# Kernel tuning notes

Hardware: AMD Instinct MI355X
Metric: run time of the kernel (lower is better)

Reference implementation:

```python
import jax, jax.numpy as jnp
import numpy as np

BLOCK_DIM = 32
INPUT_DIM = 1024
N_BLOCKS = INPUT_DIM // BLOCK_DIM  # 32
HIDDEN = 2 * BLOCK_DIM             # 64
GAPS = [1, 32]                     # block_dim**i for i in range(num_layers=2)


def setup_inputs() -> dict:
    key = jax.random.key(0)
    ks = jax.random.split(key, 9)
    s = 1.0 / np.sqrt(BLOCK_DIM)
    sh = 1.0 / np.sqrt(HIDDEN)
    return {
        "x": jax.random.normal(ks[0], (16384, INPUT_DIM), dtype=jnp.float32),
        # facto net 0: BlockLinear(32, 32, 64) -> ELU -> BlockLinear(32, 64, 32)
        "W1a": jax.random.uniform(ks[1], (N_BLOCKS, BLOCK_DIM, HIDDEN), jnp.float32, -s, s),
        "b1a": jax.random.uniform(ks[2], (N_BLOCKS, HIDDEN), jnp.float32, -s, s),
        "W2a": jax.random.uniform(ks[3], (N_BLOCKS, HIDDEN, BLOCK_DIM), jnp.float32, -sh, sh),
        "b2a": jax.random.uniform(ks[4], (N_BLOCKS, BLOCK_DIM), jnp.float32, -sh, sh),
        # facto net 1
        "W1b": jax.random.uniform(ks[5], (N_BLOCKS, BLOCK_DIM, HIDDEN), jnp.float32, -s, s),
        "b1b": jax.random.uniform(ks[6], (N_BLOCKS, HIDDEN), jnp.float32, -s, s),
        "W2b": jax.random.uniform(ks[7], (N_BLOCKS, HIDDEN, BLOCK_DIM), jnp.float32, -sh, sh),
        "b2b": jax.random.uniform(ks[8], (N_BLOCKS, BLOCK_DIM), jnp.float32, -sh, sh),
    }


def _block_res_mlp(x, W1, b1, W2, b2):
    # x: (bs, input_dim) -> (n_blocks, bs, block_dim)
    bs = x.shape[0]
    xb = x.reshape(bs, N_BLOCKS, BLOCK_DIM).transpose(1, 0, 2)
    h = jax.nn.elu(jnp.einsum('nbi,nio->nbo', xb, W1) + b1[:, None, :])
    h = jnp.einsum('nbi,nio->nbo', h, W2) + b2[:, None, :]
    yb = h + xb  # residual
    return yb.transpose(1, 0, 2).reshape(bs, -1)


def reference(x, W1a, b1a, W2a, b2a, W1b, b1b, W2b, b2b):
    bs = x.shape[0]
    params = [(W1a, b1a, W2a, b2a), (W1b, b1b, W2b, b2b)]
    y = x
    for gap, (W1, b1, W2, b2) in zip(GAPS, params):
        # strided mixing permutation before the block MLP
        y = y.reshape(-1, BLOCK_DIM, gap).transpose(0, 2, 1).reshape(bs, -1)
        y = _block_res_mlp(y, W1, b1, W2, b2)
        # inverse permutation
        y = y.reshape(-1, gap, BLOCK_DIM).transpose(0, 2, 1)
    return y.reshape(bs, -1)
```

## Files before the change

### kernel.cpp

```cpp
#include <hip/hip_runtime.h>


typedef unsigned short u16t;
typedef __bf16 bf16x8 __attribute__((ext_vector_type(8)));
typedef __bf16 bf16x4 __attribute__((ext_vector_type(4)));
typedef float f32x4 __attribute__((ext_vector_type(4)));

__device__ __forceinline__ u16t f2b(float f) {
  union { float f; unsigned u; } v; v.f = f;
  unsigned r = v.u + 0x7FFFu + ((v.u >> 16) & 1u);
  return (u16t)(r >> 16);
}
__device__ __forceinline__ float b2f(u16t h) {
  union { unsigned u; float f; } v; v.u = ((unsigned)h) << 16;
  return v.f;
}
__device__ __forceinline__ u16t f2b_hw(float f) {
  union { __bf16 h; u16t u; } v; v.h = (__bf16)f;
  return v.u;
}
__device__ __forceinline__ float elu(float v) {
  return fmaxf(v, 0.f) + fminf(__expf(v) - 1.f, 0.f);
}

__device__ __forceinline__ int swz(int idx) {
  return idx ^ ((((idx >> 6) ^ (idx >> 10)) & 15) << 2);
}

__global__ __launch_bounds__(256) void pack_weights(
    const float* __restrict__ W1a, const float* __restrict__ W2a,
    const float* __restrict__ W1b, const float* __restrict__ W2b,
    u16t* __restrict__ pW1, u16t* __restrict__ pW2) {
  int tidg = blockIdx.x * 256 + threadIdx.x;
  int tensor = tidg >> 14;
  int r  = tidg & 16383;
  int L  = r >> 13;
  int r2 = r & 8191;
  int n    = r2 >> 8;
  int f    = (r2 >> 6) & 3;
  int lane = r2 & 63;
  int q = lane >> 4, t = lane & 15;

  union { u16t us[8]; uint4 v; } w;
  if (tensor == 0) {
    const float* src = L ? W1b : W1a;
#pragma unroll
    for (int j = 0; j < 8; j++)
      w.us[j] = f2b(src[n * 2048 + (q * 8 + j) * 64 + f * 16 + t]);
    *(uint4*)(pW1 + (size_t)((((L * 32 + n) * 4 + f) * 64 + lane) * 8)) = w.v;
  } else {
    const float* src = L ? W2b : W2a;
    int e = f >> 1, c2 = f & 1;
#pragma unroll
    for (int j = 0; j < 8; j++) {
      int feat = 32 * e + (j >= 4 ? 16 : 0) + 4 * q + (j & 3);
      w.us[j] = f2b(src[n * 2048 + feat * 32 + 16 * c2 + t]);
    }
    *(uint4*)(pW2 + (size_t)((((L * 32 + n) * 4 + f) * 64 + lane) * 8)) = w.v;
  }
}

template <int L>
__device__ __forceinline__ void compute_layer(
    const bf16x8* __restrict__ afr, u16t* __restrict__ tile,
    const u16t* __restrict__ pW1, const u16t* __restrict__ pW2,
    const float* __restrict__ b1, const float* __restrict__ b2,
    int n0, int lane, int q, int t, const bf16x8* __restrict__ ifr) {
#pragma unroll
  for (int u = 0; u < 8; u++) {
    const int n = n0 + u;
    const int wbase = ((L * 32 + n) * 4) * 512 + lane * 8;

    bf16x8 bfrag[2];
#pragma unroll
    for (int e = 0; e < 2; e++) {
      bf16x8 w1lo = *(const bf16x8*)(pW1 + wbase + (2 * e) * 512);
      bf16x8 w1hi = *(const bf16x8*)(pW1 + wbase + (2 * e + 1) * 512);
      f32x4 b1lo = *(const f32x4*)(b1 + n * 64 + (2 * e) * 16 + q * 4);
      f32x4 b1hi = *(const f32x4*)(b1 + n * 64 + (2 * e + 1) * 16 + q * 4);
      f32x4 h0 = __builtin_amdgcn_mfma_f32_16x16x32_bf16(w1lo, afr[u], b1lo, 0, 0, 0);
      f32x4 h1 = __builtin_amdgcn_mfma_f32_16x16x32_bf16(w1hi, afr[u], b1hi, 0, 0, 0);
      bf16x4 a0, a1;
#pragma unroll
      for (int r = 0; r < 4; r++) {
        a0[r] = (__bf16)elu(h0[r]);
        a1[r] = (__bf16)elu(h1[r]);
      }
      bfrag[e] = __builtin_shufflevector(a0, a1, 0, 1, 2, 3, 4, 5, 6, 7);
    }

#pragma unroll
    for (int c2 = 0; c2 < 2; c2++) {
      f32x4 b2v = *(const f32x4*)(b2 + n * 32 + c2 * 16 + q * 4);
      f32x4 acc = __builtin_amdgcn_mfma_f32_16x16x32_bf16(ifr[c2], afr[u], b2v, 0, 0, 0);
#pragma unroll
      for (int e = 0; e < 2; e++) {
        bf16x8 w2f = *(const bf16x8*)(pW2 + wbase + (e * 2 + c2) * 512);
        acc = __builtin_amdgcn_mfma_f32_16x16x32_bf16(w2f, bfrag[e], acc, 0, 0, 0);
      }
#pragma unroll
      for (int r = 0; r < 4; r++) {
        int cc  = c2 * 16 + q * 4 + r;
        int idx = cc * 512 + t * 32 + n;
        tile[swz(idx)] = f2b_hw(acc[r]);
      }
    }
  }
}

__global__ __launch_bounds__(256, 2) void mixer_kernel(
    const float* __restrict__ x,
    const float* __restrict__ b1a, const float* __restrict__ b2a,
    const float* __restrict__ b1b, const float* __restrict__ b2b,
    const u16t* __restrict__ pW1, const u16t* __restrict__ pW2,
    float* __restrict__ out) {
  __shared__ u16t tile[16384];

  const int tid  = threadIdx.x;
  const int wave = tid >> 6, lane = tid & 63;
  const int q = lane >> 4, t = lane & 15;
  const int r0 = blockIdx.x * 16;
  const int n0 = wave * 8;

  bf16x8 ifr[2];
#pragma unroll
  for (int c2 = 0; c2 < 2; c2++) {
    union { u16t us[8]; bf16x8 v; } w;
#pragma unroll
    for (int j = 0; j < 8; j++)
      w.us[j] = ((q * 8 + j) == (c2 * 16 + t)) ? (u16t)0x3F80 : (u16t)0;
    ifr[c2] = w.v;
  }

  bf16x8 afr[8];
#pragma unroll
  for (int u = 0; u < 8; u++) {
    const float* gp = x + (size_t)(r0 + t) * 1024 + (n0 + u) * 32 + q * 8;
    float4 v0 = *(const float4*)gp;
    float4 v1 = *(const float4*)(gp + 4);
    union { __bf16 h[8]; bf16x8 v; } a;
    a.h[0] = (__bf16)v0.x; a.h[1] = (__bf16)v0.y; a.h[2] = (__bf16)v0.z; a.h[3] = (__bf16)v0.w;
    a.h[4] = (__bf16)v1.x; a.h[5] = (__bf16)v1.y; a.h[6] = (__bf16)v1.z; a.h[7] = (__bf16)v1.w;
    afr[u] = a.v;
  }

  compute_layer<0>(afr, tile, pW1, pW2, b1a, b2a, n0, lane, q, t, ifr);
  __syncthreads();

#pragma unroll
  for (int u = 0; u < 8; u++) {
    const int n2 = n0 + u;
    int idx = n2 * 512 + t * 32 + q * 8;
    union { ushort4 h[2]; bf16x8 v; } a;
    a.h[0] = *(const ushort4*)&tile[swz(idx)];
    a.h[1] = *(const ushort4*)&tile[swz(idx + 4)];
    afr[u] = a.v;
  }
  __syncthreads();

  compute_layer<1>(afr, tile, pW1, pW2, b1b, b2b, n0, lane, q, t, ifr);
  __syncthreads();

#pragma unroll
  for (int i = 0; i < 16; i++) {
    int c  = tid >> 3;
    int n2 = (tid & 7) * 4;
    int idx = c * 512 + i * 32 + n2;
    ushort4 hv = *(const ushort4*)&tile[swz(idx)];
    float4 o;
    o.x = b2f(hv.x); o.y = b2f(hv.y); o.z = b2f(hv.z); o.w = b2f(hv.w);
    *(float4*)(out + (size_t)(r0 + i) * 1024 + tid * 4) = o;
  }
}

extern "C" void kernel_launch(void* const* d_in, const int* in_sizes, int n_in,
                              void* d_out, int out_size, void* d_ws, size_t ws_size,
                              hipStream_t stream) {
  const float* x   = (const float*)d_in[0];
  const float* W1a = (const float*)d_in[1];
  const float* b1a = (const float*)d_in[2];
  const float* W2a = (const float*)d_in[3];
  const float* b2a = (const float*)d_in[4];
  const float* W1b = (const float*)d_in[5];
  const float* b1b = (const float*)d_in[6];
  const float* W2b = (const float*)d_in[7];
  const float* b2b = (const float*)d_in[8];
  float* out = (float*)d_out;

  u16t* pW1 = (u16t*)d_ws;
  u16t* pW2 = pW1 + 131072;

  const int rows = in_sizes[0] / 1024;

  pack_weights<<<128, 256, 0, stream>>>(W1a, W2a, W1b, W2b, pW1, pW2);
  mixer_kernel<<<rows / 16, 256, 0, stream>>>(x, b1a, b2a, b1b, b2b, pW1, pW2, out);
}
```

Baseline: 162.4 us.

## Process 32 rows per block with 8 waves and stage input via LDS

```diff
diff --git a/kernel.cpp b/kernel.cpp
--- a/kernel.cpp
+++ b/kernel.cpp
@@ -60,67 +60,93 @@
   }
 }
 
+__device__ __forceinline__ void gather_afr(bf16x8* __restrict__ afr,
+                                           const u16t* __restrict__ tile,
+                                           int w0, int q, int t) {
+#pragma unroll
+  for (int b = 0; b < 4; b++) {
+#pragma unroll
+    for (int rg = 0; rg < 2; rg++) {
+      const int n = w0 + b;
+      const int row = rg * 16 + t;
+      const int idx = n * 1024 + row * 32 + q * 8;
+      union { ushort4 h[2]; bf16x8 v; } a;
+      a.h[0] = *(const ushort4*)&tile[swz(idx)];
+      a.h[1] = *(const ushort4*)&tile[swz(idx + 4)];
+      afr[b * 2 + rg] = a.v;
+    }
+  }
+}
+
 template <int L>
 __device__ __forceinline__ void compute_layer(
     const bf16x8* __restrict__ afr, u16t* __restrict__ tile,
     const u16t* __restrict__ pW1, const u16t* __restrict__ pW2,
     const float* __restrict__ b1, const float* __restrict__ b2,
-    int n0, int lane, int q, int t, const bf16x8* __restrict__ ifr) {
-#pragma unroll
-  for (int u = 0; u < 8; u++) {
-    const int n = n0 + u;
+    int w0, int lane, int q, int t, const bf16x8* __restrict__ ifr) {
+#pragma unroll
+  for (int b = 0; b < 4; b++) {
+    const int n = w0 + b;
     const int wbase = ((L * 32 + n) * 4) * 512 + lane * 8;
 
-    bf16x8 bfrag[2];
-#pragma unroll
-    for (int e = 0; e < 2; e++) {
-      bf16x8 w1lo = *(const bf16x8*)(pW1 + wbase + (2 * e) * 512);
-      bf16x8 w1hi = *(const bf16x8*)(pW1 + wbase + (2 * e + 1) * 512);
-      f32x4 b1lo = *(const f32x4*)(b1 + n * 64 + (2 * e) * 16 + q * 4);
-      f32x4 b1hi = *(const f32x4*)(b1 + n * 64 + (2 * e + 1) * 16 + q * 4);
-      f32x4 h0 = __builtin_amdgcn_mfma_f32_16x16x32_bf16(w1lo, afr[u], b1lo, 0, 0, 0);
-      f32x4 h1 = __builtin_amdgcn_mfma_f32_16x16x32_bf16(w1hi, afr[u], b1hi, 0, 0, 0);
-      bf16x4 a0, a1;
-#pragma unroll
-      for (int r = 0; r < 4; r++) {
-        a0[r] = (__bf16)elu(h0[r]);
-        a1[r] = (__bf16)elu(h1[r]);
+    bf16x8 w1f[4], w2f[4];
+#pragma unroll
+    for (int f = 0; f < 4; f++) {
+      w1f[f] = *(const bf16x8*)(pW1 + wbase + f * 512);
+      w2f[f] = *(const bf16x8*)(pW2 + wbase + f * 512);
+    }
+
+#pragma unroll
+    for (int rg = 0; rg < 2; rg++) {
+      const bf16x8 a = afr[b * 2 + rg];
+
+      bf16x8 bfrag[2];
+#pragma unroll
+      for (int e = 0; e < 2; e++) {
+        f32x4 b1lo = *(const f32x4*)(b1 + n * 64 + (2 * e) * 16 + q * 4);
+        f32x4 b1hi = *(const f32x4*)(b1 + n * 64 + (2 * e + 1) * 16 + q * 4);
+        f32x4 h0 = __builtin_amdgcn_mfma_f32_16x16x32_bf16(w1f[2 * e],     a, b1lo, 0, 0, 0);
+        f32x4 h1 = __builtin_amdgcn_mfma_f32_16x16x32_bf16(w1f[2 * e + 1], a, b1hi, 0, 0, 0);
+        bf16x4 a0, a1;
+#pragma unroll
+        for (int r = 0; r < 4; r++) {
+          a0[r] = (__bf16)elu(h0[r]);
+          a1[r] = (__bf16)elu(h1[r]);
+        }
+        bfrag[e] = __builtin_shufflevector(a0, a1, 0, 1, 2, 3, 4, 5, 6, 7);
       }
-      bfrag[e] = __builtin_shufflevector(a0, a1, 0, 1, 2, 3, 4, 5, 6, 7);
-    }
-
-#pragma unroll
-    for (int c2 = 0; c2 < 2; c2++) {
-      f32x4 b2v = *(const f32x4*)(b2 + n * 32 + c2 * 16 + q * 4);
-      f32x4 acc = __builtin_amdgcn_mfma_f32_16x16x32_bf16(ifr[c2], afr[u], b2v, 0, 0, 0);
-#pragma unroll
-      for (int e = 0; e < 2; e++) {
-        bf16x8 w2f = *(const bf16x8*)(pW2 + wbase + (e * 2 + c2) * 512);
-        acc = __builtin_amdgcn_mfma_f32_16x16x32_bf16(w2f, bfrag[e], acc, 0, 0, 0);
+
+#pragma unroll
+      for (int c2 = 0; c2 < 2; c2++) {
+        f32x4 b2v = *(const f32x4*)(b2 + n * 32 + c2 * 16 + q * 4);
+        f32x4 acc = __builtin_amdgcn_mfma_f32_16x16x32_bf16(ifr[c2], a, b2v, 0, 0, 0);
+#pragma unroll
+        for (int e = 0; e < 2; e++)
+          acc = __builtin_amdgcn_mfma_f32_16x16x32_bf16(w2f[e * 2 + c2], bfrag[e], acc, 0, 0, 0);
+#pragma unroll
+        for (int r = 0; r < 4; r++) {
+          int cc  = c2 * 16 + q * 4 + r;
+          int idx = cc * 1024 + (rg * 16 + t) * 32 + n;
+          tile[swz(idx)] = f2b_hw(acc[r]);
+        }
       }
-#pragma unroll
-      for (int r = 0; r < 4; r++) {
-        int cc  = c2 * 16 + q * 4 + r;
-        int idx = cc * 512 + t * 32 + n;
-        tile[swz(idx)] = f2b_hw(acc[r]);
-      }
-    }
-  }
-}
-
-__global__ __launch_bounds__(256, 2) void mixer_kernel(
+    }
+  }
+}
+
+__global__ __launch_bounds__(512, 2) void mixer_kernel(
     const float* __restrict__ x,
     const float* __restrict__ b1a, const float* __restrict__ b2a,
     const float* __restrict__ b1b, const float* __restrict__ b2b,
     const u16t* __restrict__ pW1, const u16t* __restrict__ pW2,
     float* __restrict__ out) {
-  __shared__ u16t tile[16384];
+  __shared__ u16t tile[32768];
 
   const int tid  = threadIdx.x;
   const int wave = tid >> 6, lane = tid & 63;
   const int q = lane >> 4, t = lane & 15;
-  const int r0 = blockIdx.x * 16;
-  const int n0 = wave * 8;
+  const int r0 = blockIdx.x * 32;
+  const int w0 = wave * 4;
 
   bf16x8 ifr[2];
 #pragma unroll
@@ -132,44 +158,38 @@
     ifr[c2] = w.v;
   }
 
+#pragma unroll
+  for (int i = 0; i < 16; i++) {
+    int e = i * 512 + tid;
+    int row = e >> 8, c4 = e & 255;
+    float4 v = *(const float4*)(x + (size_t)(r0 + row) * 1024 + c4 * 4);
+    ushort4 hv;
+    hv.x = f2b_hw(v.x); hv.y = f2b_hw(v.y); hv.z = f2b_hw(v.z); hv.w = f2b_hw(v.w);
+    int idx = (c4 >> 3) * 1024 + row * 32 + 4 * (c4 & 7);
+    *(ushort4*)&tile[swz(idx)] = hv;
+  }
+  __syncthreads();
+
   bf16x8 afr[8];
-#pragma unroll
-  for (int u = 0; u < 8; u++) {
-    const float* gp = x + (size_t)(r0 + t) * 1024 + (n0 + u) * 32 + q * 8;
-    float4 v0 = *(const float4*)gp;
-    float4 v1 = *(const float4*)(gp + 4);
-    union { __bf16 h[8]; bf16x8 v; } a;
-    a.h[0] = (__bf16)v0.x; a.h[1] = (__bf16)v0.y; a.h[2] = (__bf16)v0.z; a.h[3] = (__bf16)v0.w;
-    a.h[4] = (__bf16)v1.x; a.h[5] = (__bf16)v1.y; a.h[6] = (__bf16)v1.z; a.h[7] = (__bf16)v1.w;
-    afr[u] = a.v;
-  }
-
-  compute_layer<0>(afr, tile, pW1, pW2, b1a, b2a, n0, lane, q, t, ifr);
-  __syncthreads();
-
-#pragma unroll
-  for (int u = 0; u < 8; u++) {
-    const int n2 = n0 + u;
-    int idx = n2 * 512 + t * 32 + q * 8;
-    union { ushort4 h[2]; bf16x8 v; } a;
-    a.h[0] = *(const ushort4*)&tile[swz(idx)];
-    a.h[1] = *(const ushort4*)&tile[swz(idx + 4)];
-    afr[u] = a.v;
-  }
-  __syncthreads();
-
-  compute_layer<1>(afr, tile, pW1, pW2, b1b, b2b, n0, lane, q, t, ifr);
+  gather_afr(afr, tile, w0, q, t);
+  __syncthreads();
+  compute_layer<0>(afr, tile, pW1, pW2, b1a, b2a, w0, lane, q, t, ifr);
+  __syncthreads();
+
+  gather_afr(afr, tile, w0, q, t);
+  __syncthreads();
+  compute_layer<1>(afr, tile, pW1, pW2, b1b, b2b, w0, lane, q, t, ifr);
   __syncthreads();
 
 #pragma unroll
   for (int i = 0; i < 16; i++) {
-    int c  = tid >> 3;
-    int n2 = (tid & 7) * 4;
-    int idx = c * 512 + i * 32 + n2;
+    int e = i * 512 + tid;
+    int row = e >> 8, g = e & 255;
+    int idx = (g >> 3) * 1024 + row * 32 + 4 * (g & 7);
     ushort4 hv = *(const ushort4*)&tile[swz(idx)];
     float4 o;
     o.x = b2f(hv.x); o.y = b2f(hv.y); o.z = b2f(hv.z); o.w = b2f(hv.w);
-    *(float4*)(out + (size_t)(r0 + i) * 1024 + tid * 4) = o;
+    *(float4*)(out + (size_t)(r0 + row) * 1024 + 4 * g) = o;
   }
 }
 
@@ -193,5 +213,5 @@
   const int rows = in_sizes[0] / 1024;
 
   pack_weights<<<128, 256, 0, stream>>>(W1a, W2a, W1b, W2b, pW1, pW2);
-  mixer_kernel<<<rows / 16, 256, 0, stream>>>(x, b1a, b2a, b1b, b2b, pW1, pW2, out);
-}
+  mixer_kernel<<<rows / 32, 512, 0, stream>>>(x, b1a, b2a, b1b, b2b, pW1, pW2, out);
+}
```

Result: no change. 161.3 us (-0.7%).
